# Kernel optimization log

Measured on AMD Instinct MI355X. Metric: run time of the kernel, lower is better.

Reference implementation:

```python
import jax, jax.numpy as jnp
import numpy as np

N_VOXELS = 200000
DIM = 96
KVOL = 343  # 7^3 depthwise kernel offsets
N_EDGES = 3200000


def setup_inputs() -> dict:
    key = jax.random.key(0)
    ks = jax.random.split(key, 10)
    feats = jax.random.normal(ks[0], (N_VOXELS, DIM), dtype=jnp.float32)
    w_dw = jax.random.normal(ks[1], (KVOL, DIM), dtype=jnp.float32) * 0.02
    b_dw = jax.random.normal(ks[2], (DIM,), dtype=jnp.float32) * 0.02
    ln_w = jnp.ones((DIM,), dtype=jnp.float32)
    ln_b = jnp.zeros((DIM,), dtype=jnp.float32)
    w1 = jax.random.normal(ks[3], (DIM, 4 * DIM), dtype=jnp.float32) * 0.02
    b1 = jax.random.normal(ks[4], (4 * DIM,), dtype=jnp.float32) * 0.02
    w2 = jax.random.normal(ks[5], (4 * DIM, DIM), dtype=jnp.float32) * 0.02
    b2 = jax.random.normal(ks[6], (DIM,), dtype=jnp.float32) * 0.02
    in_idx = jax.random.randint(ks[7], (N_EDGES,), 0, N_VOXELS, dtype=jnp.int32)
    out_idx = jax.random.randint(ks[8], (N_EDGES,), 0, N_VOXELS, dtype=jnp.int32)
    kernel_idx = jax.random.randint(ks[9], (N_EDGES,), 0, KVOL, dtype=jnp.int32)
    return {"feats": feats, "w_dw": w_dw, "b_dw": b_dw, "ln_w": ln_w,
            "ln_b": ln_b, "w1": w1, "b1": b1, "w2": w2, "b2": b2,
            "in_idx": in_idx, "out_idx": out_idx, "kernel_idx": kernel_idx}


def reference(feats, w_dw, b_dw, ln_w, ln_b, w1, b1, w2, b2,
              in_idx, out_idx, kernel_idx):
    n = feats.shape[0]
    # sparse depthwise conv via kernel-map gather/scatter:
    # out[o, c] += feats[i, c] * w_dw[k, c] for each edge (i, o, k)
    contrib = feats[in_idx] * w_dw[kernel_idx]           # [E, C]
    x = jax.ops.segment_sum(contrib, out_idx, num_segments=n) + b_dw
    # LayerNorm over channels, eps=1e-6
    mu = jnp.mean(x, axis=-1, keepdims=True)
    var = jnp.mean(jnp.square(x - mu), axis=-1, keepdims=True)
    x = (x - mu) * jax.lax.rsqrt(var + 1e-6) * ln_w + ln_b
    # pointwise MLP with exact GELU
    h = jax.nn.gelu(x @ w1 + b1, approximate=False)      # [N, 4C]
    x = h @ w2 + b2                                      # [N, C]
    # residual (drop_path rate 0.0 -> identity)
    return feats + x
```

## Files before the change

kernel.cpp:

```cpp
#include <hip/hip_runtime.h>
#include <hip/hip_bf16.h>

#define NVOX 200000
#define DIM 96
#define KVOL 343
#define NEDGE 3200000
#define HID 384
#define TM 32
#define SLOT_CAP 64

typedef __attribute__((ext_vector_type(8))) __bf16 bf16x8;
typedef __attribute__((ext_vector_type(4))) __bf16 bf16x4;
typedef __attribute__((ext_vector_type(4))) float f32x4;
typedef __attribute__((ext_vector_type(4))) int i32x4;

__global__ void zero_cnt(int* __restrict__ cnt) {
    int i = blockIdx.x * 256 + threadIdx.x;
    if (i < NVOX) cnt[i] = 0;
}

__global__ void prep_scatter(const float* __restrict__ feats, const float* __restrict__ w1,
                             const float* __restrict__ w2, const float* __restrict__ w_dw,
                             __bf16* __restrict__ featsb, __hip_bfloat16* __restrict__ w1t,
                             __hip_bfloat16* __restrict__ w2t, __bf16* __restrict__ wdwb,
                             const i32x4* __restrict__ in4, const i32x4* __restrict__ out4,
                             const i32x4* __restrict__ k4, int* __restrict__ cnt,
                             unsigned* __restrict__ slots) {
    int t = blockIdx.x * 256 + threadIdx.x;
    f32x4 v = __builtin_nontemporal_load((const f32x4*)(feats + t * 4));
    bf16x4 o;
    o[0] = (__bf16)v.x; o[1] = (__bf16)v.y; o[2] = (__bf16)v.z; o[3] = (__bf16)v.w;
    __builtin_nontemporal_store(o, (bf16x4*)(featsb + t * 4));
    if (t < HID * DIM) {
        int n1 = t / DIM, k1 = t % DIM;
        w1t[t] = __float2bfloat16(w1[k1 * HID + n1]);
        int n2 = t / HID, k2 = t % HID;
        w2t[t] = __float2bfloat16(w2[k2 * DIM + n2]);
        if (t < KVOL * DIM) wdwb[t] = (__bf16)w_dw[t];
    }
    if (t < NEDGE / 4) {
        i32x4 i = __builtin_nontemporal_load(&in4[t]);
        i32x4 oo = __builtin_nontemporal_load(&out4[t]);
        i32x4 k = __builtin_nontemporal_load(&k4[t]);
        int d;
        d = atomicAdd(&cnt[oo.x], 1);
        __builtin_nontemporal_store((unsigned)i.x | ((unsigned)k.x << 18), &slots[oo.x * SLOT_CAP + d]);
        d = atomicAdd(&cnt[oo.y], 1);
        __builtin_nontemporal_store((unsigned)i.y | ((unsigned)k.y << 18), &slots[oo.y * SLOT_CAP + d]);
        d = atomicAdd(&cnt[oo.z], 1);
        __builtin_nontemporal_store((unsigned)i.z | ((unsigned)k.z << 18), &slots[oo.z * SLOT_CAP + d]);
        d = atomicAdd(&cnt[oo.w], 1);
        __builtin_nontemporal_store((unsigned)i.w | ((unsigned)k.w << 18), &slots[oo.w * SLOT_CAP + d]);
    }
}

__global__ __launch_bounds__(256, 4) void fused_all(
    const __bf16* __restrict__ featsb, const __bf16* __restrict__ wdwb,
    const float* __restrict__ b_dw,
    const float* __restrict__ ln_w, const float* __restrict__ ln_b,
    const __hip_bfloat16* __restrict__ w1t, const float* __restrict__ b1,
    const __hip_bfloat16* __restrict__ w2t, const float* __restrict__ b2,
    const unsigned* __restrict__ slots, const int* __restrict__ cnt,
    float* __restrict__ out)
{
    __shared__ __hip_bfloat16 At[TM][104];
    __shared__ __align__(16) char shb[TM * 200 * 2];
    __hip_bfloat16 (*Ht)[200] = (__hip_bfloat16 (*)[200])shb;
    unsigned (*recsL)[68] = (unsigned (*)[68])shb;

    const int t   = threadIdx.x;
    const int blk = blockIdx.x;

    {
        const int row  = t >> 3;
        const int sub  = t & 7;
        const int part = sub & 3;
        const int half = sub >> 2;
        const int c0   = part * 24;
        const int v    = blk * TM + row;

        int c = cnt[v];
        if (c > SLOT_CAP) c = SLOT_CAP;
        const unsigned* sp = slots + v * SLOT_CAP;

        if (sub * 4 < c)
            *(uint4*)&recsL[row][sub * 4] = *(const uint4*)(sp + sub * 4);
        if (32 + sub * 4 < c)
            *(uint4*)&recsL[row][32 + sub * 4] = *(const uint4*)(sp + 32 + sub * 4);
        __syncthreads();

        float xa[24];
        #pragma unroll
        for (int j = 0; j < 24; ++j) xa[j] = 0.f;

        const __bf16* fbase = featsb + c0;
        const __bf16* wbase = wdwb + c0;
        const unsigned* rl = recsL[row];

        const int e_lo = half ? (c >> 1) : 0;
        const int e_hi = half ? c : (c >> 1);

#define LDE(F, W, ee) { unsigned rr = rl[ee]; \
        const __bf16* fr = fbase + (int)(rr & 0x3FFFFu) * DIM; \
        const __bf16* wr = wbase + (int)(rr >> 18) * DIM; \
        F##0 = *(const bf16x8*)(fr);      W##0 = *(const bf16x8*)(wr); \
        F##1 = *(const bf16x8*)(fr + 8);  W##1 = *(const bf16x8*)(wr + 8); \
        F##2 = *(const bf16x8*)(fr + 16); W##2 = *(const bf16x8*)(wr + 16); }

#define ACC(F, W) { \
        _Pragma("unroll") for (int j = 0; j < 8; ++j) xa[j]      += (float)F##0[j] * (float)W##0[j]; \
        _Pragma("unroll") for (int j = 0; j < 8; ++j) xa[8 + j]  += (float)F##1[j] * (float)W##1[j]; \
        _Pragma("unroll") for (int j = 0; j < 8; ++j) xa[16 + j] += (float)F##2[j] * (float)W##2[j]; }

        bf16x8 Af0, Af1, Af2, Aw0, Aw1, Aw2, Bf0, Bf1, Bf2, Bw0, Bw1, Bw2;
        int e = e_lo;
        if (e + 2 <= e_hi) {
            LDE(Af, Aw, e); LDE(Bf, Bw, e + 1);
            e += 2;
            for (; e + 2 <= e_hi; e += 2) {
                bf16x8 Cf0, Cf1, Cf2, Cw0, Cw1, Cw2, Df0, Df1, Df2, Dw0, Dw1, Dw2;
                LDE(Cf, Cw, e); LDE(Df, Dw, e + 1);
                ACC(Af, Aw); ACC(Bf, Bw);
                Af0 = Cf0; Af1 = Cf1; Af2 = Cf2; Aw0 = Cw0; Aw1 = Cw1; Aw2 = Cw2;
                Bf0 = Df0; Bf1 = Df1; Bf2 = Df2; Bw0 = Dw0; Bw1 = Dw1; Bw2 = Dw2;
            }
            ACC(Af, Aw); ACC(Bf, Bw);
        }
        if (e < e_hi) {
            LDE(Af, Aw, e);
            ACC(Af, Aw);
        }
#undef LDE
#undef ACC

        #pragma unroll
        for (int j = 0; j < 24; ++j) xa[j] += __shfl_xor(xa[j], 4);

        float s = 0.f, s2 = 0.f;
        #pragma unroll
        for (int j = 0; j < 24; ++j) {
            float x = xa[j] + b_dw[c0 + j];
            xa[j] = x;
            s += x; s2 += x * x;
        }
        s  += __shfl_xor(s, 1);  s  += __shfl_xor(s, 2);
        s2 += __shfl_xor(s2, 1); s2 += __shfl_xor(s2, 2);
        float mean = s * (1.f / 96.f);
        float var  = s2 * (1.f / 96.f) - mean * mean;
        float rstd = rsqrtf(var + 1e-6f);

        if (half == 0) {
            #pragma unroll
            for (int jj = 0; jj < 3; ++jj) {
                bf16x8 pack;
                #pragma unroll
                for (int j = 0; j < 8; ++j) {
                    int cch = c0 + jj*8 + j;
                    float xn = (xa[jj*8+j] - mean) * rstd * ln_w[cch] + ln_b[cch];
                    pack[j] = (__bf16)xn;
                }
                *(bf16x8*)&At[row][c0 + jj*8] = pack;
            }
        }
    }
    __syncthreads();

    const int w  = t >> 6;
    const int l  = t & 63;
    const int lr = l & 15;
    const int lk = l >> 4;
    const int rb = w >> 1;
    const int jh = w & 1;

    f32x4 acc2[3];
    #pragma unroll
    for (int j = 0; j < 3; ++j) acc2[j] = (f32x4){0.f, 0.f, 0.f, 0.f};

    #pragma unroll
    for (int h = 0; h < 2; ++h) {
        f32x4 acc[6];
        #pragma unroll
        for (int j = 0; j < 6; ++j) acc[j] = (f32x4){0.f, 0.f, 0.f, 0.f};

        #pragma unroll
        for (int kk = 0; kk < 3; ++kk) {
            bf16x8 a = *(const bf16x8*)&At[rb*16 + lr][kk*32 + lk*8];
            #pragma unroll
            for (int j = 0; j < 6; ++j) {
                int col = h*192 + jh*96 + j*16 + lr;
                bf16x8 b = *(const bf16x8*)&w1t[col * DIM + kk*32 + lk*8];
                acc[j] = __builtin_amdgcn_mfma_f32_16x16x32_bf16(a, b, acc[j], 0, 0, 0);
            }
        }

        if (h == 1) __syncthreads();

        #pragma unroll
        for (int j = 0; j < 6; ++j) {
            int col = h*192 + jh*96 + j*16 + lr;
            float bb = b1[col];
            #pragma unroll
            for (int r = 0; r < 4; ++r) {
                float vv = acc[j][r] + bb;
                float ge = 0.5f * vv * (1.f + erff(vv * 0.70710678f));
                Ht[rb*16 + lk*4 + r][jh*96 + j*16 + lr] = __float2bfloat16(ge);
            }
        }
        __syncthreads();

        #pragma unroll
        for (int kk = 0; kk < 6; ++kk) {
            bf16x8 a = *(const bf16x8*)&Ht[rb*16 + lr][kk*32 + lk*8];
            #pragma unroll
            for (int j = 0; j < 3; ++j) {
                int col = jh*48 + j*16 + lr;
                bf16x8 b = *(const bf16x8*)&w2t[col * HID + (h*6 + kk)*32 + lk*8];
                acc2[j] = __builtin_amdgcn_mfma_f32_16x16x32_bf16(a, b, acc2[j], 0, 0, 0);
            }
        }
    }

    #pragma unroll
    for (int j = 0; j < 3; ++j) {
        int col = jh*48 + j*16 + lr;
        float bb = b2[col];
        #pragma unroll
        for (int r = 0; r < 4; ++r) {
            int grow = blk * TM + rb*16 + lk*4 + r;
            int off = grow * DIM + col;
            float res = (float)featsb[off];
            __builtin_nontemporal_store(acc2[j][r] + bb + res, &out[off]);
        }
    }
}

extern "C" void kernel_launch(void* const* d_in, const int* in_sizes, int n_in,
                              void* d_out, int out_size, void* d_ws, size_t ws_size,
                              hipStream_t stream) {
    const float* feats = (const float*)d_in[0];
    const float* w_dw  = (const float*)d_in[1];
    const float* b_dw  = (const float*)d_in[2];
    const float* ln_w  = (const float*)d_in[3];
    const float* ln_b  = (const float*)d_in[4];
    const float* w1    = (const float*)d_in[5];
    const float* b1    = (const float*)d_in[6];
    const float* w2    = (const float*)d_in[7];
    const float* b2    = (const float*)d_in[8];
    const int* in_idx  = (const int*)d_in[9];
    const int* out_idx = (const int*)d_in[10];
    const int* k_idx   = (const int*)d_in[11];
    float* out = (float*)d_out;

    char* ws = (char*)d_ws;
    unsigned* slots = (unsigned*)ws;
    int* cnt   = (int*)(ws + 51200000);
    __hip_bfloat16* w1t = (__hip_bfloat16*)(ws + 52000000);
    __hip_bfloat16* w2t = (__hip_bfloat16*)(ws + 52073728);
    __bf16* wdwb = (__bf16*)(ws + 52147456);
    __bf16* featsb = (__bf16*)(ws + 52213312);

    zero_cnt<<<(NVOX + 255) / 256, 256, 0, stream>>>(cnt);
    prep_scatter<<<(NVOX * DIM / 4) / 256, 256, 0, stream>>>(
        feats, w1, w2, w_dw, featsb, w1t, w2t, wdwb,
        (const i32x4*)in_idx, (const i32x4*)out_idx, (const i32x4*)k_idx, cnt, slots);
    fused_all<<<NVOX / TM, 256, 0, stream>>>(featsb, wdwb, b_dw, ln_w, ln_b,
                                             w1t, b1, w2t, b2, slots, cnt, out);
}
```

Baseline: 545.0 us.

## Transpose edge slot buckets to slot-major layout and split scatter kernel

Edge records go into a slot-major array (slot d, voxel v) instead of voxel-major buckets of 64, so neighbouring voxels' records for the same slot sit next to each other. Counter zeroing moves into the prep kernel, and the edge scatter becomes its own kernel that runs after prep. Overflow writes past SLOT_CAP are now skipped. The intent is to reduce scattered write traffic and partial-line writes in the scatter, at the cost of the fused kernel loading records with strided scalar reads instead of 16-byte vector loads.

New measurement: 477.7 us. -12.4%, faster.

```diff
diff --git a/kernel.cpp b/kernel.cpp
--- a/kernel.cpp
+++ b/kernel.cpp
@@ -14,18 +14,11 @@
 typedef __attribute__((ext_vector_type(4))) float f32x4;
 typedef __attribute__((ext_vector_type(4))) int i32x4;
 
-__global__ void zero_cnt(int* __restrict__ cnt) {
-    int i = blockIdx.x * 256 + threadIdx.x;
-    if (i < NVOX) cnt[i] = 0;
-}
-
-__global__ void prep_scatter(const float* __restrict__ feats, const float* __restrict__ w1,
-                             const float* __restrict__ w2, const float* __restrict__ w_dw,
-                             __bf16* __restrict__ featsb, __hip_bfloat16* __restrict__ w1t,
-                             __hip_bfloat16* __restrict__ w2t, __bf16* __restrict__ wdwb,
-                             const i32x4* __restrict__ in4, const i32x4* __restrict__ out4,
-                             const i32x4* __restrict__ k4, int* __restrict__ cnt,
-                             unsigned* __restrict__ slots) {
+__global__ void prep(const float* __restrict__ feats, const float* __restrict__ w1,
+                     const float* __restrict__ w2, const float* __restrict__ w_dw,
+                     __bf16* __restrict__ featsb, __hip_bfloat16* __restrict__ w1t,
+                     __hip_bfloat16* __restrict__ w2t, __bf16* __restrict__ wdwb,
+                     int* __restrict__ cnt) {
     int t = blockIdx.x * 256 + threadIdx.x;
     f32x4 v = __builtin_nontemporal_load((const f32x4*)(feats + t * 4));
     bf16x4 o;
@@ -38,20 +31,25 @@
         w2t[t] = __float2bfloat16(w2[k2 * DIM + n2]);
         if (t < KVOL * DIM) wdwb[t] = (__bf16)w_dw[t];
     }
-    if (t < NEDGE / 4) {
-        i32x4 i = __builtin_nontemporal_load(&in4[t]);
-        i32x4 oo = __builtin_nontemporal_load(&out4[t]);
-        i32x4 k = __builtin_nontemporal_load(&k4[t]);
-        int d;
-        d = atomicAdd(&cnt[oo.x], 1);
-        __builtin_nontemporal_store((unsigned)i.x | ((unsigned)k.x << 18), &slots[oo.x * SLOT_CAP + d]);
-        d = atomicAdd(&cnt[oo.y], 1);
-        __builtin_nontemporal_store((unsigned)i.y | ((unsigned)k.y << 18), &slots[oo.y * SLOT_CAP + d]);
-        d = atomicAdd(&cnt[oo.z], 1);
-        __builtin_nontemporal_store((unsigned)i.z | ((unsigned)k.z << 18), &slots[oo.z * SLOT_CAP + d]);
-        d = atomicAdd(&cnt[oo.w], 1);
-        __builtin_nontemporal_store((unsigned)i.w | ((unsigned)k.w << 18), &slots[oo.w * SLOT_CAP + d]);
-    }
+    if (t < NVOX) cnt[t] = 0;
+}
+
+__global__ void scatter_T(const i32x4* __restrict__ in4, const i32x4* __restrict__ out4,
+                          const i32x4* __restrict__ k4, int* __restrict__ cnt,
+                          unsigned* __restrict__ slots) {
+    int t = blockIdx.x * 256 + threadIdx.x;
+    i32x4 i = __builtin_nontemporal_load(&in4[t]);
+    i32x4 o = __builtin_nontemporal_load(&out4[t]);
+    i32x4 k = __builtin_nontemporal_load(&k4[t]);
+    int d;
+    d = atomicAdd(&cnt[o.x], 1);
+    if (d < SLOT_CAP) slots[d * NVOX + o.x] = (unsigned)i.x | ((unsigned)k.x << 18);
+    d = atomicAdd(&cnt[o.y], 1);
+    if (d < SLOT_CAP) slots[d * NVOX + o.y] = (unsigned)i.y | ((unsigned)k.y << 18);
+    d = atomicAdd(&cnt[o.z], 1);
+    if (d < SLOT_CAP) slots[d * NVOX + o.z] = (unsigned)i.z | ((unsigned)k.z << 18);
+    d = atomicAdd(&cnt[o.w], 1);
+    if (d < SLOT_CAP) slots[d * NVOX + o.w] = (unsigned)i.w | ((unsigned)k.w << 18);
 }
 
 __global__ __launch_bounds__(256, 4) void fused_all(
@@ -81,12 +79,9 @@
 
         int c = cnt[v];
         if (c > SLOT_CAP) c = SLOT_CAP;
-        const unsigned* sp = slots + v * SLOT_CAP;
-
-        if (sub * 4 < c)
-            *(uint4*)&recsL[row][sub * 4] = *(const uint4*)(sp + sub * 4);
-        if (32 + sub * 4 < c)
-            *(uint4*)&recsL[row][32 + sub * 4] = *(const uint4*)(sp + 32 + sub * 4);
+
+        for (int d = sub; d < c; d += 8)
+            recsL[row][d] = slots[d * NVOX + v];
         __syncthreads();
 
         float xa[24];
@@ -259,10 +254,11 @@
     __bf16* wdwb = (__bf16*)(ws + 52147456);
     __bf16* featsb = (__bf16*)(ws + 52213312);
 
-    zero_cnt<<<(NVOX + 255) / 256, 256, 0, stream>>>(cnt);
-    prep_scatter<<<(NVOX * DIM / 4) / 256, 256, 0, stream>>>(
-        feats, w1, w2, w_dw, featsb, w1t, w2t, wdwb,
-        (const i32x4*)in_idx, (const i32x4*)out_idx, (const i32x4*)k_idx, cnt, slots);
+    prep<<<(NVOX * DIM / 4) / 256, 256, 0, stream>>>(feats, w1, w2, w_dw,
+                                                     featsb, w1t, w2t, wdwb, cnt);
+    scatter_T<<<NEDGE / 4 / 256, 256, 0, stream>>>((const i32x4*)in_idx,
+                                                   (const i32x4*)out_idx,
+                                                   (const i32x4*)k_idx, cnt, slots);
     fused_all<<<NVOX / TM, 256, 0, stream>>>(featsb, wdwb, b_dw, ln_w, ln_b,
                                              w1t, b1, w2t, b2, slots, cnt, out);
 }
```
